# Performance work log

Hardware: AMD Instinct MI355X
Metric: run time of the kernel (lower is better)

Reference implementation:

```python
import jax, jax.numpy as jnp
import numpy as np

T = 0.1        # temperature
MARGIN = 0.0   # margin m
NEG_IOU = 0.5  # negative iou threshold
K = 2          # pos_topk
WEIGHT = 1.0


def _l2norm(x, eps=1e-12):
    n = jnp.sqrt(jnp.sum(x * x, axis=-1, keepdims=True))
    return x / jnp.maximum(n, eps)


def setup_inputs() -> dict:
    key = jax.random.key(0)
    k0, k1, k2, k3 = jax.random.split(key, 4)
    B, C, N = 8, 256, 128
    s_per, m_per = 4, 2          # sentences per video, targets per sentence
    S, M = B * s_per, B * s_per * m_per
    video_feats = jax.random.normal(k0, (B, C, N, N), dtype=jnp.float32)
    sents_feats = jax.random.normal(k1, (S, C), dtype=jnp.float32)
    num_sentences = jnp.full((B,), s_per, dtype=jnp.int32)
    num_targets = jnp.full((S,), m_per, dtype=jnp.int32)
    iou2d = jax.random.uniform(k2, (S, N, N), dtype=jnp.float32)
    iou2ds = jax.random.uniform(k3, (M, N, N), dtype=jnp.float32)
    mask2d = jnp.asarray(np.triu(np.ones((N, N), dtype=bool)))
    return {"video_feats": video_feats, "sents_feats": sents_feats,
            "num_sentences": num_sentences, "num_targets": num_targets,
            "iou2d": iou2d, "iou2ds": iou2ds, "mask2d": mask2d}


def reference(video_feats, sents_feats, num_sentences, num_targets, iou2d, iou2ds, mask2d):
    B, C, N, _ = video_feats.shape
    S = iou2d.shape[0]
    M = iou2ds.shape[0]
    P = N * (N + 1) // 2  # number of valid proposals in upper-triangular mask2d
    flat_idx = jnp.nonzero(mask2d.reshape(-1), size=P)[0]

    # masked_select -> (B, P, C) proposal features, l2-normalized over C
    vf = video_feats.reshape(B, C, N * N)[:, :, flat_idx].transpose(0, 2, 1)
    vf = _l2norm(vf)
    sf = _l2norm(sents_feats)  # normalized as in original (unused downstream)
    iou2d_p = iou2d.reshape(S, -1)[:, flat_idx]    # (S, P)
    iou2ds_p = iou2ds.reshape(M, -1)[:, flat_idx]  # (M, P)

    s_per = S // B  # uniform sentences per video (static)
    m_per = M // S  # uniform targets per sentence (static)
    scatter_s2v = jnp.repeat(jnp.arange(B), s_per)    # (S,)
    scatter_m2s = jnp.repeat(jnp.arange(S), m_per)    # (M,)
    scatter_m2v = scatter_s2v[scatter_m2s]            # (M,)

    # top-K proposals per target moment by iou2ds
    topk_idx = jax.lax.top_k(iou2ds_p, K)[1]  # (M, K)
    topk_feats = jnp.take_along_axis(vf[scatter_m2v], topk_idx[:, :, None], axis=1)  # (M,K,C)
    pos_feats = topk_feats.reshape(M * K, C)

    # all (ref, pos) pairs within each sentence's m_per*K selected proposals
    mK = m_per * K
    a = jnp.arange(mK)
    shifts = jnp.arange(S) * mK
    ref_idx = (shifts[:, None] + jnp.repeat(a, mK)[None, :]).reshape(-1)  # (E,)
    pos_idx = (shifts[:, None] + jnp.tile(a, mK)[None, :]).reshape(-1)    # (E,)
    scatter_e2s = jnp.repeat(jnp.arange(S), mK * mK)                      # (E,)

    intra_pos = jnp.sum(pos_feats[ref_idx] * pos_feats[pos_idx], axis=-1)  # (E,)
    intra_all = pos_feats @ vf.reshape(-1, C).T                            # (M*K, B*P)

    # neg mask: within own video, exclude proposals with iou > NEG_IOU; other videos all negative
    own = scatter_s2v[:, None] == jnp.arange(B)[None, :]                   # (S, B)
    pos_mask = (own[:, :, None] & (iou2d_p > NEG_IOU)[:, None, :]).reshape(S, B * P)
    neg_mask = ~pos_mask

    ps = intra_pos
    all_s = intra_all[ref_idx]           # (E, B*P)
    nm = neg_mask[scatter_e2s]           # (E, B*P)
    pos_exp = jnp.exp((ps - MARGIN) / T)
    neg_sum = jnp.sum(jnp.exp(all_s / T) * nm, axis=-1)
    loss = jnp.mean(-((ps - MARGIN) / T - jnp.log(pos_exp + neg_sum)))
    return loss * WEIGHT
```

## Files before the change

kernel.cpp:

```cpp
#include <hip/hip_runtime.h>
#include <math.h>

#define NN    128
#define NN2   16384
#define CDIM  256
#define BV    8
#define MM    64
#define RR    128
#define PP    8256
#define NBLK  1032
#define BPB   129
#define TEMP  0.1f
#define NEGIOU 0.5f

typedef __attribute__((ext_vector_type(8))) short bf16x8;
typedef __attribute__((ext_vector_type(4))) float f32x4;

static __device__ __forceinline__ unsigned short f2bf(float x) {
    union { float f; unsigned u; } c; c.f = x;
    unsigned r = c.u + 0x7FFFu + ((c.u >> 16) & 1u);
    return (unsigned short)(r >> 16);
}

__global__ __launch_bounds__(256) void topk_part_kernel(const float* __restrict__ iou2ds,
                                                        float* __restrict__ pv,
                                                        int* __restrict__ pk) {
    int m = blockIdx.x, q = blockIdx.y, tid = threadIdx.x;
    const float* src = iou2ds + (size_t)m * NN2;
    float v1 = -1e30f, v2 = -1e30f;
    int k1 = 0x7fffffff, k2 = 0x7fffffff;
    int base = q * 4096;
#pragma unroll
    for (int i = 0; i < 16; ++i) {
        int k = base + tid + 256 * i;
        int r = k >> 7, c = k & 127;
        if (c < r) continue;
        float v = src[k];
        if (v > v1 || (v == v1 && k < k1)) { v2 = v1; k2 = k1; v1 = v; k1 = k; }
        else if (v > v2 || (v == v2 && k < k2)) { v2 = v; k2 = k; }
    }
    __shared__ float sv[512];  __shared__ int sk[512];
    __shared__ float sv2[128]; __shared__ int sk2[128];
    sv[tid * 2] = v1; sv[tid * 2 + 1] = v2;
    sk[tid * 2] = k1; sk[tid * 2 + 1] = k2;
    __syncthreads();
    if (tid < 64) {
        float b1 = -1e30f, b2 = -1e30f; int c1 = 0x7fffffff, c2 = 0x7fffffff;
        for (int t = tid * 8; t < tid * 8 + 8; ++t) {
            float v = sv[t]; int k = sk[t];
            if (v > b1 || (v == b1 && k < c1)) { b2 = b1; c2 = c1; b1 = v; c1 = k; }
            else if (v > b2 || (v == b2 && k < c2)) { b2 = v; c2 = k; }
        }
        sv2[tid * 2] = b1; sv2[tid * 2 + 1] = b2;
        sk2[tid * 2] = c1; sk2[tid * 2 + 1] = c2;
    }
    __syncthreads();
    if (tid == 0) {
        float b1 = -1e30f, b2 = -1e30f; int c1 = 0x7fffffff, c2 = 0x7fffffff;
        for (int t = 0; t < 128; ++t) {
            float v = sv2[t]; int k = sk2[t];
            if (v > b1 || (v == b1 && k < c1)) { b2 = b1; c2 = c1; b1 = v; c1 = k; }
            else if (v > b2 || (v == b2 && k < c2)) { b2 = v; c2 = k; }
        }
        pv[(m * 4 + q) * 2] = b1; pv[(m * 4 + q) * 2 + 1] = b2;
        pk[(m * 4 + q) * 2] = c1; pk[(m * 4 + q) * 2 + 1] = c2;
    }
}

__global__ __launch_bounds__(64) void posfeat_kernel(const float* __restrict__ vfeat,
                                                     const float* __restrict__ pv,
                                                     const int* __restrict__ pk,
                                                     float* __restrict__ pos,
                                                     unsigned short* __restrict__ posFrag) {
    int r = blockIdx.x, lane = threadIdx.x;
    int m = r >> 1, b = m >> 3, kk = r & 1;
    float b1 = -1e30f, b2 = -1e30f; int c1 = 0x7fffffff, c2 = 0x7fffffff;
    for (int t = 0; t < 8; ++t) {
        float v = pv[m * 8 + t]; int k = pk[m * 8 + t];
        if (v > b1 || (v == b1 && k < c1)) { b2 = b1; c2 = c1; b1 = v; c1 = k; }
        else if (v > b2 || (v == b2 && k < c2)) { b2 = v; c2 = k; }
    }
    int ij = kk ? c2 : c1;
    const float* base = vfeat + (size_t)b * CDIM * NN2 + ij;
    float v[4];
    float ss = 0.0f;
#pragma unroll
    for (int q = 0; q < 4; ++q) {
        int c = lane + 64 * q;
        v[q] = base[(size_t)c * NN2];
        ss += v[q] * v[q];
    }
#pragma unroll
    for (int o = 32; o > 0; o >>= 1) ss += __shfl_xor(ss, o, 64);
    float inv = 1.0f / fmaxf(sqrtf(ss), 1e-12f);
#pragma unroll
    for (int q = 0; q < 4; ++q) {
        int c = lane + 64 * q;
        float val = v[q] * inv;
        pos[r * CDIM + c] = val;
        int idx = (((c >> 5) * 8 + (r >> 4)) * 64 + ((r & 15) | (((c >> 3) & 3) << 4))) * 8 + (c & 7);
        posFrag[idx] = f2bf(val);
    }
}

__global__ __launch_bounds__(512, 4) void neg_kernel(const float* __restrict__ vfeat,
                                                     const float* __restrict__ iou2d,
                                                     const unsigned short* __restrict__ posFrag,
                                                     float* __restrict__ part) {
    __shared__ unsigned short sB[2][2][4][64][8];
    __shared__ int   sIJ[64];
    __shared__ int   sMask[64];
    __shared__ float sNP[8][64];
    __shared__ float sInv[64];
    __shared__ float sNeg[RR];

    int tid = threadIdx.x;
    int bid = blockIdx.x;
    int b   = bid / BPB;
    int p0  = (bid - b * BPB) * 64;

    if (tid < RR) sNeg[tid] = 0.0f;
    if (tid < 64) {
        int p = p0 + tid;
        int i = (int)((257.0f - sqrtf(66049.0f - 8.0f * (float)p)) * 0.5f);
        if (i < 0) i = 0;
        while ((i + 1) * (257 - (i + 1)) / 2 <= p) ++i;
        while (i * (257 - i) / 2 > p) --i;
        int j = p - i * (257 - i) / 2 + i;
        int ij = i * NN + j;
        sIJ[tid] = ij;
        int mask = 0;
#pragma unroll
        for (int t = 0; t < 4; ++t) {
            float iv = iou2d[((size_t)(4 * b + t)) * NN2 + ij];
            mask |= (iv > NEGIOU) ? (1 << t) : 0;
        }
        sMask[tid] = mask;
    }

    int lane = tid & 63;
    int col  = tid & 63;
    int wv   = tid >> 6;
    int rowgroup = wv >> 1;
    int colgroup = wv & 1;

    bf16x8 afrag[2][8];
    const bf16x8* pf = (const bf16x8*)posFrag;
#pragma unroll
    for (int mt = 0; mt < 2; ++mt)
#pragma unroll
        for (int s = 0; s < 8; ++s)
            afrag[mt][s] = pf[(s * 8 + rowgroup * 2 + mt) * 64 + lane];

    __syncthreads();

    const float* vcol = vfeat + (size_t)b * CDIM * NN2 + sIJ[col];

    f32x4 acc[2][2];
#pragma unroll
    for (int mt = 0; mt < 2; ++mt)
#pragma unroll
        for (int nt = 0; nt < 2; ++nt)
#pragma unroll
            for (int e = 0; e < 4; ++e) acc[mt][nt][e] = 0.0f;

    float nrm = 0.0f;
    float r[8];
#pragma unroll
    for (int j = 0; j < 8; ++j) r[j] = vcol[(size_t)(wv * 8 + j) * NN2];

    int s_loc = wv >> 2;
    int slot  = (col & 15) | ((wv & 3) << 4);
    int nt_w  = col >> 4;

    for (int ph = 0; ph < 4; ++ph) {
        union { bf16x8 v; unsigned u[4]; } pkd;
#pragma unroll
        for (int j = 0; j < 4; ++j)
            pkd.u[j] = (unsigned)f2bf(r[2 * j]) | ((unsigned)f2bf(r[2 * j + 1]) << 16);
#pragma unroll
        for (int j = 0; j < 8; ++j) nrm = fmaf(r[j], r[j], nrm);
        *(bf16x8*)&sB[ph & 1][s_loc][nt_w][slot][0] = pkd.v;
        __syncthreads();
        if (ph < 3) {
#pragma unroll
            for (int j = 0; j < 8; ++j)
                r[j] = vcol[(size_t)((ph + 1) * 64 + wv * 8 + j) * NN2];
        }
#pragma unroll
        for (int s = 0; s < 2; ++s)
#pragma unroll
            for (int ntl = 0; ntl < 2; ++ntl) {
                bf16x8 bfrag = *(const bf16x8*)&sB[ph & 1][s][colgroup * 2 + ntl][lane][0];
#pragma unroll
                for (int mt = 0; mt < 2; ++mt)
                    acc[mt][ntl] = __builtin_amdgcn_mfma_f32_16x16x32_bf16(
                        afrag[mt][ph * 2 + s], bfrag, acc[mt][ntl], 0, 0, 0);
            }
    }

    sNP[wv][col] = nrm;
    __syncthreads();
    if (tid < 64) {
        float s = 0.0f;
        for (int t = 0; t < 8; ++t) s += sNP[t][tid];
        sInv[tid] = 10.0f / fmaxf(sqrtf(s), 1e-12f);
    }
    __syncthreads();

#pragma unroll
    for (int mt = 0; mt < 2; ++mt)
#pragma unroll
        for (int ntl = 0; ntl < 2; ++ntl)
#pragma unroll
            for (int reg = 0; reg < 4; ++reg) {
                int row = rowgroup * 32 + mt * 16 + ((lane >> 4) << 2) + reg;
                int cl  = colgroup * 32 + ntl * 16 + (lane & 15);
                float e = __expf(acc[mt][ntl][reg] * sInv[cl]);
                int excl = ((row >> 4) == b) & ((sMask[cl] >> ((row >> 2) & 3)) & 1);
                e = excl ? 0.0f : e;
#pragma unroll
                for (int off = 1; off < 16; off <<= 1) e += __shfl_xor(e, off, 64);
                if ((lane & 15) == 0) atomicAdd(&sNeg[row], e);
            }
    __syncthreads();
    if (tid < RR) part[(size_t)tid * NBLK + bid] = sNeg[tid];
}

__global__ __launch_bounds__(256) void reduce_kernel(const float* __restrict__ part,
                                                     float* __restrict__ neg) {
    int r = blockIdx.x, tid = threadIdx.x;
    const float* row = part + (size_t)r * NBLK;
    float s = 0.0f;
    for (int t = tid; t < NBLK; t += 256) s += row[t];
#pragma unroll
    for (int o = 32; o > 0; o >>= 1) s += __shfl_xor(s, o, 64);
    __shared__ float sw[4];
    if ((tid & 63) == 0) sw[tid >> 6] = s;
    __syncthreads();
    if (tid == 0) neg[r] = sw[0] + sw[1] + sw[2] + sw[3];
}

__global__ __launch_bounds__(256) void loss_kernel(const float* __restrict__ pos,
                                                   const float* __restrict__ neg,
                                                   float* __restrict__ out) {
    int tid = threadIdx.x;
    float local = 0.0f;
    for (int e = tid; e < 512; e += 256) {
        int s  = e >> 4;
        int aa = (e >> 2) & 3;
        int bb = e & 3;
        int rr = s * 4 + aa;
        int pp = s * 4 + bb;
        const float4* pr = (const float4*)(pos + rr * CDIM);
        const float4* pq = (const float4*)(pos + pp * CDIM);
        float dot = 0.0f;
        for (int c = 0; c < CDIM / 4; ++c) {
            float4 a = pr[c], bv = pq[c];
            dot += a.x * bv.x + a.y * bv.y + a.z * bv.z + a.w * bv.w;
        }
        float x = dot / TEMP;
        local += logf(__expf(x) + neg[rr]) - x;
    }
#pragma unroll
    for (int o = 32; o > 0; o >>= 1) local += __shfl_xor(local, o, 64);
    __shared__ float sred[4];
    if ((tid & 63) == 0) sred[tid >> 6] = local;
    __syncthreads();
    if (tid == 0) out[0] = (sred[0] + sred[1] + sred[2] + sred[3]) / 512.0f;
}

extern "C" void kernel_launch(void* const* d_in, const int* in_sizes, int n_in,
                              void* d_out, int out_size, void* d_ws, size_t ws_size,
                              hipStream_t stream) {
    (void)in_sizes; (void)n_in; (void)out_size; (void)ws_size;
    const float* vfeat  = (const float*)d_in[0];
    const float* iou2d  = (const float*)d_in[4];
    const float* iou2ds = (const float*)d_in[5];

    float* ws = (float*)d_ws;
    float*          pos     = ws;
    unsigned short* posFrag = (unsigned short*)(ws + 32768);
    float*          pv      = ws + 32768 + 16384;
    int*            pk      = (int*)(pv + 512);
    float*          part    = pv + 1024;
    float*          neg     = part + RR * NBLK;

    topk_part_kernel<<<dim3(MM, 4), 256, 0, stream>>>(iou2ds, pv, pk);
    posfeat_kernel  <<<RR, 64, 0, stream>>>(vfeat, pv, pk, pos, posFrag);
    neg_kernel      <<<NBLK, 512, 0, stream>>>(vfeat, iou2d, posFrag, part);
    reduce_kernel   <<<RR, 256, 0, stream>>>(part, neg);
    loss_kernel     <<<1, 256, 0, stream>>>(pos, neg, (float*)d_out);
}
```

Measured before the change: 256.8 us.

## Fuse top-k and positive feature gather; stream A fragments per phase; transpose partials

Merges the two-stage top-k and the positive-feature normalization into one kernel of 64 blocks, each scanning a full iou map and then gathering its two proposals. This removes one launch and the intermediate partial buffers. The neg kernel now loads A fragments per phase instead of holding all 16 in registers, which lowers register pressure and may help occupancy. Partial sums are stored block-major so neg_kernel's writes are contiguous, while reduce_kernel's reads become strided. The fused top-k uses only 64 blocks, so its serial scan is less parallel than before.

```diff
diff --git a/kernel.cpp b/kernel.cpp
--- a/kernel.cpp
+++ b/kernel.cpp
@@ -22,25 +22,26 @@
     return (unsigned short)(r >> 16);
 }
 
-__global__ __launch_bounds__(256) void topk_part_kernel(const float* __restrict__ iou2ds,
-                                                        float* __restrict__ pv,
-                                                        int* __restrict__ pk) {
-    int m = blockIdx.x, q = blockIdx.y, tid = threadIdx.x;
+__global__ __launch_bounds__(256) void pos_kernel(const float* __restrict__ iou2ds,
+                                                  const float* __restrict__ vfeat,
+                                                  float* __restrict__ pos,
+                                                  unsigned short* __restrict__ posFrag) {
+    int m = blockIdx.x, tid = threadIdx.x;
     const float* src = iou2ds + (size_t)m * NN2;
     float v1 = -1e30f, v2 = -1e30f;
     int k1 = 0x7fffffff, k2 = 0x7fffffff;
-    int base = q * 4096;
-#pragma unroll
-    for (int i = 0; i < 16; ++i) {
-        int k = base + tid + 256 * i;
-        int r = k >> 7, c = k & 127;
-        if (c < r) continue;
+#pragma unroll 4
+    for (int i = 0; i < 64; ++i) {
+        int k = tid + 256 * i;
+        int rr = k >> 7, cc = k & 127;
+        if (cc < rr) continue;
         float v = src[k];
         if (v > v1 || (v == v1 && k < k1)) { v2 = v1; k2 = k1; v1 = v; k1 = k; }
         else if (v > v2 || (v == v2 && k < k2)) { v2 = v; k2 = k; }
     }
     __shared__ float sv[512];  __shared__ int sk[512];
     __shared__ float sv2[128]; __shared__ int sk2[128];
+    __shared__ int sIdx[2];
     sv[tid * 2] = v1; sv[tid * 2 + 1] = v2;
     sk[tid * 2] = k1; sk[tid * 2 + 1] = k2;
     __syncthreads();
@@ -62,44 +63,34 @@
             if (v > b1 || (v == b1 && k < c1)) { b2 = b1; c2 = c1; b1 = v; c1 = k; }
             else if (v > b2 || (v == b2 && k < c2)) { b2 = v; c2 = k; }
         }
-        pv[(m * 4 + q) * 2] = b1; pv[(m * 4 + q) * 2 + 1] = b2;
-        pk[(m * 4 + q) * 2] = c1; pk[(m * 4 + q) * 2 + 1] = c2;
-    }
-}
-
-__global__ __launch_bounds__(64) void posfeat_kernel(const float* __restrict__ vfeat,
-                                                     const float* __restrict__ pv,
-                                                     const int* __restrict__ pk,
-                                                     float* __restrict__ pos,
-                                                     unsigned short* __restrict__ posFrag) {
-    int r = blockIdx.x, lane = threadIdx.x;
-    int m = r >> 1, b = m >> 3, kk = r & 1;
-    float b1 = -1e30f, b2 = -1e30f; int c1 = 0x7fffffff, c2 = 0x7fffffff;
-    for (int t = 0; t < 8; ++t) {
-        float v = pv[m * 8 + t]; int k = pk[m * 8 + t];
-        if (v > b1 || (v == b1 && k < c1)) { b2 = b1; c2 = c1; b1 = v; c1 = k; }
-        else if (v > b2 || (v == b2 && k < c2)) { b2 = v; c2 = k; }
-    }
-    int ij = kk ? c2 : c1;
-    const float* base = vfeat + (size_t)b * CDIM * NN2 + ij;
-    float v[4];
-    float ss = 0.0f;
-#pragma unroll
-    for (int q = 0; q < 4; ++q) {
-        int c = lane + 64 * q;
-        v[q] = base[(size_t)c * NN2];
-        ss += v[q] * v[q];
-    }
-#pragma unroll
-    for (int o = 32; o > 0; o >>= 1) ss += __shfl_xor(ss, o, 64);
-    float inv = 1.0f / fmaxf(sqrtf(ss), 1e-12f);
-#pragma unroll
-    for (int q = 0; q < 4; ++q) {
-        int c = lane + 64 * q;
-        float val = v[q] * inv;
-        pos[r * CDIM + c] = val;
-        int idx = (((c >> 5) * 8 + (r >> 4)) * 64 + ((r & 15) | (((c >> 3) & 3) << 4))) * 8 + (c & 7);
-        posFrag[idx] = f2bf(val);
+        sIdx[0] = c1; sIdx[1] = c2;
+    }
+    __syncthreads();
+
+    int wv = tid >> 6, lane = tid & 63;
+    if (wv < 2) {
+        int r = m * 2 + wv;
+        int b = m >> 3;
+        const float* base = vfeat + (size_t)b * CDIM * NN2 + sIdx[wv];
+        float v[4];
+        float ss = 0.0f;
+#pragma unroll
+        for (int q = 0; q < 4; ++q) {
+            int c = lane + 64 * q;
+            v[q] = base[(size_t)c * NN2];
+            ss += v[q] * v[q];
+        }
+#pragma unroll
+        for (int o = 32; o > 0; o >>= 1) ss += __shfl_xor(ss, o, 64);
+        float inv = 1.0f / fmaxf(sqrtf(ss), 1e-12f);
+#pragma unroll
+        for (int q = 0; q < 4; ++q) {
+            int c = lane + 64 * q;
+            float val = v[q] * inv;
+            pos[r * CDIM + c] = val;
+            int idx = (((c >> 5) * 8 + (r >> 4)) * 64 + ((r & 15) | (((c >> 3) & 3) << 4))) * 8 + (c & 7);
+            posFrag[idx] = f2bf(val);
+        }
     }
 }
 
@@ -144,13 +135,7 @@
     int rowgroup = wv >> 1;
     int colgroup = wv & 1;
 
-    bf16x8 afrag[2][8];
     const bf16x8* pf = (const bf16x8*)posFrag;
-#pragma unroll
-    for (int mt = 0; mt < 2; ++mt)
-#pragma unroll
-        for (int s = 0; s < 8; ++s)
-            afrag[mt][s] = pf[(s * 8 + rowgroup * 2 + mt) * 64 + lane];
 
     __syncthreads();
 
@@ -173,7 +158,15 @@
     int slot  = (col & 15) | ((wv & 3) << 4);
     int nt_w  = col >> 4;
 
+#pragma unroll
     for (int ph = 0; ph < 4; ++ph) {
+        bf16x8 af[2][2];
+#pragma unroll
+        for (int s = 0; s < 2; ++s)
+#pragma unroll
+            for (int mt = 0; mt < 2; ++mt)
+                af[s][mt] = pf[((ph * 2 + s) * 8 + rowgroup * 2 + mt) * 64 + lane];
+
         union { bf16x8 v; unsigned u[4]; } pkd;
 #pragma unroll
         for (int j = 0; j < 4; ++j)
@@ -195,7 +188,7 @@
 #pragma unroll
                 for (int mt = 0; mt < 2; ++mt)
                     acc[mt][ntl] = __builtin_amdgcn_mfma_f32_16x16x32_bf16(
-                        afrag[mt][ph * 2 + s], bfrag, acc[mt][ntl], 0, 0, 0);
+                        af[s][mt], bfrag, acc[mt][ntl], 0, 0, 0);
             }
     }
 
@@ -224,15 +217,14 @@
                 if ((lane & 15) == 0) atomicAdd(&sNeg[row], e);
             }
     __syncthreads();
-    if (tid < RR) part[(size_t)tid * NBLK + bid] = sNeg[tid];
+    if (tid < RR) part[(size_t)bid * RR + tid] = sNeg[tid];
 }
 
 __global__ __launch_bounds__(256) void reduce_kernel(const float* __restrict__ part,
                                                      float* __restrict__ neg) {
     int r = blockIdx.x, tid = threadIdx.x;
-    const float* row = part + (size_t)r * NBLK;
     float s = 0.0f;
-    for (int t = tid; t < NBLK; t += 256) s += row[t];
+    for (int t = tid; t < NBLK; t += 256) s += part[(size_t)t * RR + r];
 #pragma unroll
     for (int o = 32; o > 0; o >>= 1) s += __shfl_xor(s, o, 64);
     __shared__ float sw[4];
@@ -281,14 +273,11 @@
     float* ws = (float*)d_ws;
     float*          pos     = ws;
     unsigned short* posFrag = (unsigned short*)(ws + 32768);
-    float*          pv      = ws + 32768 + 16384;
-    int*            pk      = (int*)(pv + 512);
-    float*          part    = pv + 1024;
-    float*          neg     = part + RR * NBLK;
-
-    topk_part_kernel<<<dim3(MM, 4), 256, 0, stream>>>(iou2ds, pv, pk);
-    posfeat_kernel  <<<RR, 64, 0, stream>>>(vfeat, pv, pk, pos, posFrag);
-    neg_kernel      <<<NBLK, 512, 0, stream>>>(vfeat, iou2d, posFrag, part);
-    reduce_kernel   <<<RR, 256, 0, stream>>>(part, neg);
-    loss_kernel     <<<1, 256, 0, stream>>>(pos, neg, (float*)d_out);
-}
+    float*          part    = ws + 32768 + 16384;
+    float*          neg     = part + (size_t)RR * NBLK;
+
+    pos_kernel   <<<MM, 256, 0, stream>>>(iou2ds, vfeat, pos, posFrag);
+    neg_kernel   <<<NBLK, 512, 0, stream>>>(vfeat, iou2d, posFrag, part);
+    reduce_kernel<<<RR, 256, 0, stream>>>(part, neg);
+    loss_kernel  <<<1, 256, 0, stream>>>(pos, neg, (float*)d_out);
+}
```

Measured after the change: 275.5 us. 7.3% more time.
